# Optimization experiments

Hardware: AMD Instinct MI355X
Metric: run time of the kernel (lower is better)

The kernel has to match this reference:

```python
import jax, jax.numpy as jnp
import numpy as np

HIDDEN = 1024
KEY_DIM = 1280


def setup_inputs() -> dict:
    key = jax.random.key(0)
    ks = jax.random.split(key, 8)
    B, L = 32, 2048
    # Xavier-uniform style init for weights, bias = 0.01 (as in module)
    def xavier(k, shape):
        fan_in, fan_out = shape[1], shape[0]
        limit = float(np.sqrt(6.0 / (fan_in + fan_out)))
        return jax.random.uniform(k, shape, jnp.float32, -limit, limit)
    return {
        "query": jax.random.normal(ks[0], (B, HIDDEN), jnp.float32),
        "keys": jax.random.normal(ks[1], (B, L, KEY_DIM), jnp.float32),
        "W1_w": xavier(ks[2], (HIDDEN, HIDDEN)),
        "W1_b": jnp.full((HIDDEN,), 0.01, jnp.float32),
        "W2_w": xavier(ks[3], (HIDDEN, KEY_DIM)),
        "W2_b": jnp.full((HIDDEN,), 0.01, jnp.float32),
        "Va_w": xavier(ks[4], (1, HIDDEN)),
        "Va_b": jnp.full((1,), 0.01, jnp.float32),
    }


def reference(query, keys, W1_w, W1_b, W2_w, W2_b, Va_w, Va_b):
    # hidden: [B, H], encoder: [B, L, H]
    hidden = query @ W1_w.T + W1_b
    encoder = jnp.einsum("blk,hk->blh", keys, W2_w) + W2_b
    # additive score: Va(relu(hidden[:,None,:] + encoder)) -> [B, L]
    act = jax.nn.relu(hidden[:, None, :] + encoder)
    scores = jnp.einsum("blh,h->bl", act, Va_w[0]) + Va_b[0]
    weights = jax.nn.softmax(scores, axis=1)  # [B, L]
    context = jnp.einsum("blk,bl->bk", keys, weights)  # [B, KEY_DIM]
    return context, weights
```

## Files before the change

### kernel.cpp

```cpp
#include <hip/hip_runtime.h>
#include <hip/hip_bf16.h>
#include <cstdint>
#include <cstddef>

#define NB 32
#define NL 2048
#define NH 1024
#define NK 1280

typedef __bf16 bf16x8 __attribute__((ext_vector_type(8)));
typedef short short8 __attribute__((ext_vector_type(8)));
typedef float f32x4 __attribute__((ext_vector_type(4)));
typedef unsigned short u16x4 __attribute__((ext_vector_type(4)));
typedef unsigned short u16x8 __attribute__((ext_vector_type(8)));

__device__ __forceinline__ float bfbits2f(unsigned short b) {
    union { unsigned int u; float f; } v;
    v.u = ((unsigned int)b) << 16;
    return v.f;
}

__device__ __forceinline__ void load_lds16(const void* g, void* l) {
    __builtin_amdgcn_global_load_lds((const __attribute__((address_space(1))) void*)g,
                                     (__attribute__((address_space(3))) void*)l, 16, 0, 0);
}

__global__ __launch_bounds__(256) void k_w2cvt(const float* __restrict__ w2,
                                               unsigned short* __restrict__ w2b) {
    int i = (blockIdx.x * 256 + threadIdx.x) * 4;
    f32x4 v = *(const f32x4*)(w2 + i);
    u16x4 o;
#pragma unroll
    for (int c = 0; c < 4; ++c) {
        __bf16 b = (__bf16)v[c];
        o[c] = __builtin_bit_cast(unsigned short, b);
    }
    *(u16x4*)(w2b + i) = o;
}

__global__ __launch_bounds__(256) void k_keyscvt(const float* __restrict__ keys,
                                                 unsigned short* __restrict__ kb) {
    size_t i = ((size_t)blockIdx.x * 256 + threadIdx.x) * 8;
    f32x4 v0 = *(const f32x4*)(keys + i);
    f32x4 v1 = *(const f32x4*)(keys + i + 4);
    u16x8 o;
#pragma unroll
    for (int c = 0; c < 4; ++c) {
        o[c] = __builtin_bit_cast(unsigned short, (__bf16)v0[c]);
        o[c + 4] = __builtin_bit_cast(unsigned short, (__bf16)v1[c]);
    }
    *(u16x8*)(kb + i) = o;
}

__global__ __launch_bounds__(256) void k_hidden(const float* __restrict__ q,
                                                const float* __restrict__ w1,
                                                const float* __restrict__ w1b,
                                                const float* __restrict__ w2b,
                                                float* __restrict__ hidden) {
    const int t = threadIdx.x;
    const int h = blockIdx.x;
    __shared__ __align__(16) float w[1024];
    __shared__ float red[256];
    *(f32x4*)&w[t * 4] = *(const f32x4*)(w1 + (size_t)h * 1024 + t * 4);
    __syncthreads();
    const int b = t & 31, seg = t >> 5;
    const f32x4* q4 = (const f32x4*)(q + (size_t)b * 1024 + seg * 128);
    f32x4 accv = (f32x4){0.f, 0.f, 0.f, 0.f};
#pragma unroll 4
    for (int i = 0; i < 32; ++i) {
        f32x4 qv = q4[i];
        f32x4 wv = *(f32x4*)&w[seg * 128 + i * 4];
#pragma unroll
        for (int c = 0; c < 4; ++c) accv[c] = fmaf(qv[c], wv[c], accv[c]);
    }
    red[t] = accv[0] + accv[1] + accv[2] + accv[3];
    __syncthreads();
    if (t < 32) {
        float tot = 0.f;
#pragma unroll
        for (int sg = 0; sg < 8; ++sg) tot += red[sg * 32 + t];
        hidden[(size_t)t * 1024 + h] = tot + w1b[h] + w2b[h];
    }
}

__global__ __launch_bounds__(512, 2) void k_score_bf(const unsigned short* __restrict__ keysbf,
                                                     const unsigned short* __restrict__ w2bf,
                                                     const float* __restrict__ hidden,
                                                     const float* __restrict__ va,
                                                     float* __restrict__ spart) {
    __shared__ __align__(16) __bf16 As[32768];
    __shared__ __align__(16) __bf16 Bs[32768];
    __shared__ float sred[1024];

    const int t = threadIdx.x;
    const int lane = t & 63, wid = t >> 6;
    const int wr = wid >> 2, wc = wid & 3;
    const int pl = lane >> 4, r0 = lane & 15;

    const int bid = blockIdx.x;
    const int v = (bid & 7) * 128 + (bid >> 3);
    const int rt = v >> 2;
    const int ht = v & 3;

    const int b = rt >> 3;
    float hv[4], vav[4];
#pragma unroll
    for (int n = 0; n < 4; ++n) {
        int h = ht * 256 + wc * 64 + n * 16 + r0;
        hv[n] = hidden[(size_t)b * 1024 + h];
        vav[n] = va[h];
    }

    const int cj0 = wid * 2, cj1 = wid * 2 + 1;
    const unsigned short* pA0 = keysbf + (size_t)(rt * 256 + (cj0 & 3) * 64 + lane) * 1280 + (cj0 >> 2) * 8;
    const unsigned short* pA1 = keysbf + (size_t)(rt * 256 + (cj1 & 3) * 64 + lane) * 1280 + (cj1 >> 2) * 8;
    const unsigned short* pB0 = w2bf + (size_t)(ht * 256 + (cj0 & 3) * 64 + lane) * 1280 + (cj0 >> 2) * 8;
    const unsigned short* pB1 = w2bf + (size_t)(ht * 256 + (cj1 & 3) * 64 + lane) * 1280 + (cj1 >> 2) * 8;
    const int dst0 = cj0 * 1024 + lane * 16;
    const int dst1 = cj1 * 1024 + lane * 16;

    const int aBase = pl * 2048 + (wr * 128 + r0) * 8;
    const int bBase = pl * 2048 + (wc * 64 + r0) * 8;

    f32x4 acc[8][4];
#pragma unroll
    for (int m = 0; m < 8; ++m)
#pragma unroll
        for (int n = 0; n < 4; ++n) acc[m][n] = (f32x4){0.f, 0.f, 0.f, 0.f};
    bf16x8 bB[4];

#define ST_A(NXT, KOFF, KS)                                                          \
    do {                                                                             \
        load_lds16(pA0 + (KOFF) + (KS) * 32, (char*)As + (NXT) * 32768 + (KS) * 16384 + dst0); \
        load_lds16(pA1 + (KOFF) + (KS) * 32, (char*)As + (NXT) * 32768 + (KS) * 16384 + dst1); \
    } while (0)
#define ST_B(NXT, KOFF, KS)                                                          \
    do {                                                                             \
        load_lds16(pB0 + (KOFF) + (KS) * 32, (char*)Bs + (NXT) * 32768 + (KS) * 16384 + dst0); \
        load_lds16(pB1 + (KOFF) + (KS) * 32, (char*)Bs + (NXT) * 32768 + (KS) * 16384 + dst1); \
    } while (0)

#define PH(CUR, KS, MH, RDB, STMT, WAITN, TRAIL)                                     \
    do {                                                                             \
        if (RDB) {                                                                   \
            _Pragma("unroll") for (int n = 0; n < 4; ++n)                            \
                bB[n] = *(bf16x8*)&Bs[(CUR) * 16384 + (KS) * 8192 + bBase + n * 128];\
        }                                                                            \
        bf16x8 aT[4];                                                                \
        _Pragma("unroll") for (int mm = 0; mm < 4; ++mm)                             \
            aT[mm] = *(bf16x8*)&As[(CUR) * 16384 + (KS) * 8192 + aBase + (MH) * 512 + mm * 128]; \
        STMT;                                                                        \
        if ((WAITN) == 4) asm volatile("s_waitcnt vmcnt(4)" ::: "memory");           \
        else if ((WAITN) == 2) asm volatile("s_waitcnt vmcnt(2)" ::: "memory");      \
        else if ((WAITN) == 0) asm volatile("s_waitcnt vmcnt(0)" ::: "memory");      \
        __builtin_amdgcn_s_barrier();                                                \
        asm volatile("s_waitcnt lgkmcnt(0)" ::: "memory");                           \
        __builtin_amdgcn_sched_barrier(0);                                           \
        __builtin_amdgcn_s_setprio(1);                                               \
        _Pragma("unroll") for (int mm = 0; mm < 4; ++mm)                             \
            _Pragma("unroll") for (int n = 0; n < 4; ++n)                            \
                acc[(MH) * 4 + mm][n] = __builtin_amdgcn_mfma_f32_16x16x32_bf16(     \
                    aT[mm], bB[n], acc[(MH) * 4 + mm][n], 0, 0, 0);                  \
        __builtin_amdgcn_s_setprio(0);                                               \
        if (TRAIL) __builtin_amdgcn_s_barrier();                                     \
    } while (0)

#define TILE(CUR, NXT, KOFF, W2, W4, DOST)                                           \
    do {                                                                             \
        PH(CUR, 0, 0, 1, if (DOST) ST_A(NXT, KOFF, 0), -1, 0);                       \
        PH(CUR, 0, 1, 0, if (DOST) ST_A(NXT, KOFF, 1), W2, 0);                       \
        PH(CUR, 1, 0, 1, if (DOST) ST_B(NXT, KOFF, 0), -1, 0);                       \
        PH(CUR, 1, 1, 0, if (DOST) ST_B(NXT, KOFF, 1), W4, 1);                       \
    } while (0)

    ST_A(0, 0, 0);
    ST_A(0, 0, 1);
    ST_B(0, 0, 0);
    ST_B(0, 0, 1);
    asm volatile("s_waitcnt vmcnt(2)" ::: "memory");
    __builtin_amdgcn_s_barrier();

    int koff = 64;
    for (int t2 = 0; t2 < 9; ++t2) {
        TILE(0, 1, koff, 4, 2, 1);
        koff += 64;
        TILE(1, 0, koff, 4, 2, 1);
        koff += 64;
    }
    TILE(0, 1, koff, 4, 2, 1);
    TILE(1, 0, 0, 0, -1, 0);
#undef TILE
#undef PH
#undef ST_A
#undef ST_B

#pragma unroll
    for (int m = 0; m < 8; ++m) {
#pragma unroll
        for (int j = 0; j < 4; ++j) {
            float s = 0.f;
#pragma unroll
            for (int n = 0; n < 4; ++n) {
                float v2 = acc[m][n][j] + hv[n];
                v2 = fmaxf(v2, 0.f);
                s = fmaf(v2, vav[n], s);
            }
            s += __shfl_xor(s, 1);
            s += __shfl_xor(s, 2);
            s += __shfl_xor(s, 4);
            s += __shfl_xor(s, 8);
            if (r0 == 0) sred[(wr * 128 + m * 16 + pl * 4 + j) * 4 + wc] = s;
        }
    }
    __syncthreads();
    if (t < 256)
        spart[(size_t)ht * 65536 + rt * 256 + t] =
            (sred[t * 4] + sred[t * 4 + 1]) + (sred[t * 4 + 2] + sred[t * 4 + 3]);
}

#define LOAD_AB(IT)                                        \
    do {                                                   \
        const float* ap_ = aptr + (IT) * 32;               \
        a0 = *(const f32x4*)(ap_);                         \
        a1 = *(const f32x4*)(ap_ + 4);                     \
        a2 = *(const f32x4*)(ap_ + 8);                     \
        a3 = *(const f32x4*)(ap_ + 12);                    \
        const unsigned short* bp_ = bptr + (IT) * 32;      \
        b0 = *(const short8*)(bp_);                        \
        b1 = *(const short8*)(bp_ + 8);                    \
    } while (0)

__global__ __launch_bounds__(256, 2) void k_score_f32(const float* __restrict__ keys,
                                                      const unsigned short* __restrict__ w2bf,
                                                      const float* __restrict__ hidden,
                                                      const float* __restrict__ va,
                                                      float* __restrict__ spart) {
    __shared__ __align__(16) __bf16 As[4096];
    __shared__ __align__(16) __bf16 Bs[4096];
    __shared__ float sred[256];
    const int t = threadIdx.x;
    const int rt = blockIdx.x, ht = blockIdx.y;
    const int row = t >> 1, half = t & 1;
    const float* aptr = keys + (size_t)(rt * 128 + row) * 1280 + half * 16;
    const unsigned short* bptr = w2bf + (size_t)(ht * 128 + row) * 1280 + half * 16;
    const int wA0 = (2 * half) * 1024 + row * 8;
    const int wA1 = wA0 + 1024;
    f32x4 acc[4][4];
#pragma unroll
    for (int m = 0; m < 4; ++m)
#pragma unroll
        for (int n = 0; n < 4; ++n) acc[m][n] = (f32x4){0.f, 0.f, 0.f, 0.f};
    const int lane = t & 63, wid = t >> 6;
    const int wr = wid >> 1, wc = wid & 1;
    const int pl = lane >> 4, r0 = lane & 15;
    const int aroff = pl * 1024 + (wr * 64 + r0) * 8;
    const int broff = pl * 1024 + (wc * 64 + r0) * 8;
    f32x4 a0, a1, a2, a3;
    short8 b0, b1;
    LOAD_AB(0);
    for (int it = 0; it < 40; ++it) {
        __syncthreads();
        bf16x8 p0, p1;
#pragma unroll
        for (int e = 0; e < 4; ++e) {
            p0[e] = (__bf16)a0[e];
            p0[e + 4] = (__bf16)a1[e];
            p1[e] = (__bf16)a2[e];
            p1[e + 4] = (__bf16)a3[e];
        }
        *(bf16x8*)&As[wA0] = p0;
        *(bf16x8*)&As[wA1] = p1;
        *(short8*)&Bs[wA0] = b0;
        *(short8*)&Bs[wA1] = b1;
        __syncthreads();
        if (it + 1 < 40) LOAD_AB(it + 1);
        bf16x8 af[4], bfv[4];
#pragma unroll
        for (int m = 0; m < 4; ++m) af[m] = *(bf16x8*)&As[aroff + m * 128];
#pragma unroll
        for (int n = 0; n < 4; ++n) bfv[n] = *(bf16x8*)&Bs[broff + n * 128];
#pragma unroll
        for (int m = 0; m < 4; ++m)
#pragma unroll
            for (int n = 0; n < 4; ++n)
                acc[m][n] = __builtin_amdgcn_mfma_f32_16x16x32_bf16(af[m], bfv[n], acc[m][n], 0, 0, 0);
    }
    const int b = rt >> 4;
    float hv[4], vav[4];
#pragma unroll
    for (int n = 0; n < 4; ++n) {
        int h = ht * 128 + wc * 64 + n * 16 + r0;
        hv[n] = hidden[(size_t)b * 1024 + h];
        vav[n] = va[h];
    }
#pragma unroll
    for (int m = 0; m < 4; ++m) {
#pragma unroll
        for (int j = 0; j < 4; ++j) {
            float s = 0.f;
#pragma unroll
            for (int n = 0; n < 4; ++n) {
                float v = acc[m][n][j] + hv[n];
                v = fmaxf(v, 0.f);
                s = fmaf(v, vav[n], s);
            }
            s += __shfl_xor(s, 1);
            s += __shfl_xor(s, 2);
            s += __shfl_xor(s, 4);
            s += __shfl_xor(s, 8);
            if (r0 == 0) sred[(wr * 64 + m * 16 + pl * 4 + j) * 2 + wc] = s;
        }
    }
    __syncthreads();
    if (t < 128) spart[(size_t)ht * 65536 + rt * 128 + t] = sred[t * 2] + sred[t * 2 + 1];
}

__global__ __launch_bounds__(256) void k_softmax4(const float* __restrict__ spart,
                                                  float* __restrict__ wout) {
    const int b = blockIdx.x, t = threadIdx.x;
    __shared__ float red[256];
    float s[8];
#pragma unroll
    for (int i = 0; i < 8; ++i) {
        int l = t + i * 256;
        float v = 0.f;
#pragma unroll
        for (int ht = 0; ht < 4; ++ht) v += spart[(size_t)ht * 65536 + b * 2048 + l];
        s[i] = v;
    }
    float mx = s[0];
#pragma unroll
    for (int i = 1; i < 8; ++i) mx = fmaxf(mx, s[i]);
    red[t] = mx;
    __syncthreads();
    for (int st = 128; st > 0; st >>= 1) {
        if (t < st) red[t] = fmaxf(red[t], red[t + st]);
        __syncthreads();
    }
    mx = red[0];
    __syncthreads();
    float e[8];
    float sum = 0.f;
#pragma unroll
    for (int i = 0; i < 8; ++i) {
        e[i] = __expf(s[i] - mx);
        sum += e[i];
    }
    red[t] = sum;
    __syncthreads();
    for (int st = 128; st > 0; st >>= 1) {
        if (t < st) red[t] += red[t + st];
        __syncthreads();
    }
    float inv = 1.0f / red[0];
#pragma unroll
    for (int i = 0; i < 8; ++i) wout[(size_t)b * 2048 + t + i * 256] = e[i] * inv;
}

__global__ __launch_bounds__(256) void k_softmax8(const float* __restrict__ spart,
                                                  float* __restrict__ wout) {
    const int b = blockIdx.x, t = threadIdx.x;
    __shared__ float red[256];
    float s[8];
#pragma unroll
    for (int i = 0; i < 8; ++i) {
        int l = t + i * 256;
        float v = 0.f;
#pragma unroll
        for (int ht = 0; ht < 8; ++ht) v += spart[(size_t)ht * 65536 + b * 2048 + l];
        s[i] = v;
    }
    float mx = s[0];
#pragma unroll
    for (int i = 1; i < 8; ++i) mx = fmaxf(mx, s[i]);
    red[t] = mx;
    __syncthreads();
    for (int st = 128; st > 0; st >>= 1) {
        if (t < st) red[t] = fmaxf(red[t], red[t + st]);
        __syncthreads();
    }
    mx = red[0];
    __syncthreads();
    float e[8];
    float sum = 0.f;
#pragma unroll
    for (int i = 0; i < 8; ++i) {
        e[i] = __expf(s[i] - mx);
        sum += e[i];
    }
    red[t] = sum;
    __syncthreads();
    for (int st = 128; st > 0; st >>= 1) {
        if (t < st) red[t] += red[t + st];
        __syncthreads();
    }
    float inv = 1.0f / red[0];
#pragma unroll
    for (int i = 0; i < 8; ++i) wout[(size_t)b * 2048 + t + i * 256] = e[i] * inv;
}

__global__ __launch_bounds__(256) void k_ctx_bf(const unsigned short* __restrict__ keysbf,
                                                const float* __restrict__ wts,
                                                float* __restrict__ cpart) {
    const int b = blockIdx.x, kc = blockIdx.y, lc = blockIdx.z, t = threadIdx.x;
    const int c = t & 15, g = t >> 4;
    const unsigned short* kp = keysbf + ((size_t)b * 2048 + lc * 512 + g) * 1280 + kc * 128 + c * 8;
    const float* wb = wts + (size_t)b * 2048 + lc * 512 + g;
    float acc[8];
#pragma unroll
    for (int j = 0; j < 8; ++j) acc[j] = 0.f;
    for (int i = 0; i < 32; ++i) {
        u16x8 v = *(const u16x8*)kp;
        float w = *wb;
#pragma unroll
        for (int j = 0; j < 8; ++j) acc[j] = fmaf(w, bfbits2f(v[j]), acc[j]);
        kp += (size_t)16 * 1280;
        wb += 16;
    }
    __shared__ float sred[2048];
#pragma unroll
    for (int j = 0; j < 8; ++j) sred[t * 8 + j] = acc[j];
    __syncthreads();
    if (t < 128) {
        float s = 0.f;
#pragma unroll
        for (int g2 = 0; g2 < 16; ++g2) s += sred[g2 * 128 + t];
        cpart[((size_t)lc * 32 + b) * 1280 + kc * 128 + t] = s;
    }
}

__global__ __launch_bounds__(256) void k_ctxred4(const float* __restrict__ cpart,
                                                 float* __restrict__ ctx) {
    const int idx = blockIdx.x * 256 + threadIdx.x;
    const int b = idx / 1280, k = idx % 1280;
    float s = 0.f;
#pragma unroll
    for (int lc = 0; lc < 4; ++lc) s += cpart[((size_t)lc * 32 + b) * 1280 + k];
    ctx[(size_t)b * 1280 + k] = s;
}

__global__ __launch_bounds__(256) void k_ctxpart_f32(const float* __restrict__ keys,
                                                     const float* __restrict__ wts,
                                                     float* __restrict__ cpart) {
    const int b = blockIdx.x, lc = blockIdx.y, t = threadIdx.x;
    f32x4 acc0 = (f32x4){0.f, 0.f, 0.f, 0.f};
    f32x4 acc1 = (f32x4){0.f, 0.f, 0.f, 0.f};
    const int l0 = lc * 128;
    const float* kb = keys + ((size_t)b * 2048 + l0) * 1280;
    const float* wb = wts + (size_t)b * 2048 + l0;
    for (int l = 0; l < 128; ++l) {
        float w = wb[l];
        const f32x4* kr = (const f32x4*)(kb + (size_t)l * 1280);
        f32x4 v = kr[t];
#pragma unroll
        for (int ci = 0; ci < 4; ++ci) acc0[ci] = fmaf(v[ci], w, acc0[ci]);
        if (t < 64) {
            f32x4 v2 = kr[256 + t];
#pragma unroll
            for (int ci = 0; ci < 4; ++ci) acc1[ci] = fmaf(v2[ci], w, acc1[ci]);
        }
    }
    float* cp = cpart + ((size_t)lc * 32 + b) * 1280;
    *(f32x4*)(cp + 4 * t) = acc0;
    if (t < 64) *(f32x4*)(cp + 1024 + 4 * t) = acc1;
}

__global__ __launch_bounds__(256) void k_ctxred16(const float* __restrict__ cpart,
                                                  float* __restrict__ ctx) {
    const int idx = blockIdx.x * 256 + threadIdx.x;
    const int b = idx / 1280, k = idx % 1280;
    float s = 0.f;
#pragma unroll
    for (int lc = 0; lc < 16; ++lc) s += cpart[((size_t)lc * 32 + b) * 1280 + k];
    ctx[(size_t)b * 1280 + k] = s;
}

extern "C" void kernel_launch(void* const* d_in, const int* in_sizes, int n_in,
                              void* d_out, int out_size, void* d_ws, size_t ws_size,
                              hipStream_t stream) {
    const float* query = (const float*)d_in[0];
    const float* keys = (const float*)d_in[1];
    const float* W1_w = (const float*)d_in[2];
    const float* W1_b = (const float*)d_in[3];
    const float* W2_w = (const float*)d_in[4];
    const float* W2_b = (const float*)d_in[5];
    const float* Va_w = (const float*)d_in[6];

    float* out = (float*)d_out;
    float* ctx = out;
    float* wts = out + NB * NK;

    char* ws = (char*)d_ws;
    float* hidden = (float*)ws;
    unsigned short* w2bf = (unsigned short*)(ws + 131072);
    float* spart = (float*)(ws + 2752512);
    float* cpart = (float*)(ws + 4849664);
    unsigned short* keysbf = (unsigned short*)(ws + 7471104);
    const bool big = ws_size >= (size_t)7471104 + 167772160;

    k_w2cvt<<<1280, 256, 0, stream>>>(W2_w, w2bf);
    k_hidden<<<1024, 256, 0, stream>>>(query, W1_w, W1_b, W2_b, hidden);
    if (big) {
        k_keyscvt<<<40960, 256, 0, stream>>>(keys, keysbf);
        k_score_bf<<<1024, 512, 0, stream>>>(keysbf, w2bf, hidden, Va_w, spart);
        k_softmax4<<<32, 256, 0, stream>>>(spart, wts);
        k_ctx_bf<<<dim3(32, 10, 4), 256, 0, stream>>>(keysbf, wts, cpart);
        k_ctxred4<<<160, 256, 0, stream>>>(cpart, ctx);
    } else {
        k_score_f32<<<dim3(512, 8), 256, 0, stream>>>(keys, w2bf, hidden, Va_w, spart);
        k_softmax8<<<32, 256, 0, stream>>>(spart, wts);
        k_ctxpart_f32<<<dim3(32, 16), 256, 0, stream>>>(keys, wts, cpart);
        k_ctxred16<<<160, 256, 0, stream>>>(cpart, ctx);
    }
}
```

Baseline: 395.6 us.

## Replace four-phase barrier pipeline with one barrier per K tile

```diff
diff --git a/kernel.cpp b/kernel.cpp
--- a/kernel.cpp
+++ b/kernel.cpp
@@ -127,7 +127,6 @@
     for (int m = 0; m < 8; ++m)
 #pragma unroll
         for (int n = 0; n < 4; ++n) acc[m][n] = (f32x4){0.f, 0.f, 0.f, 0.f};
-    bf16x8 bB[4];
 
 #define ST_A(NXT, KOFF, KS)                                                          \
     do {                                                                             \
@@ -140,57 +139,64 @@
         load_lds16(pB1 + (KOFF) + (KS) * 32, (char*)Bs + (NXT) * 32768 + (KS) * 16384 + dst1); \
     } while (0)
 
-#define PH(CUR, KS, MH, RDB, STMT, WAITN, TRAIL)                                     \
+#define RD_B(DST, CUR, KS)                                                           \
+    _Pragma("unroll") for (int n = 0; n < 4; ++n)                                    \
+        DST[n] = *(bf16x8*)&Bs[(CUR) * 16384 + (KS) * 8192 + bBase + n * 128];
+#define RD_A(DST, CUR, KS, MH)                                                       \
+    _Pragma("unroll") for (int mm = 0; mm < 4; ++mm)                                 \
+        DST[mm] = *(bf16x8*)&As[(CUR) * 16384 + (KS) * 8192 + aBase + (MH) * 512 + mm * 128];
+#define MM(AV, BV, MH)                                                               \
     do {                                                                             \
-        if (RDB) {                                                                   \
-            _Pragma("unroll") for (int n = 0; n < 4; ++n)                            \
-                bB[n] = *(bf16x8*)&Bs[(CUR) * 16384 + (KS) * 8192 + bBase + n * 128];\
-        }                                                                            \
-        bf16x8 aT[4];                                                                \
-        _Pragma("unroll") for (int mm = 0; mm < 4; ++mm)                             \
-            aT[mm] = *(bf16x8*)&As[(CUR) * 16384 + (KS) * 8192 + aBase + (MH) * 512 + mm * 128]; \
-        STMT;                                                                        \
-        if ((WAITN) == 4) asm volatile("s_waitcnt vmcnt(4)" ::: "memory");           \
-        else if ((WAITN) == 2) asm volatile("s_waitcnt vmcnt(2)" ::: "memory");      \
-        else if ((WAITN) == 0) asm volatile("s_waitcnt vmcnt(0)" ::: "memory");      \
-        __builtin_amdgcn_s_barrier();                                                \
-        asm volatile("s_waitcnt lgkmcnt(0)" ::: "memory");                           \
-        __builtin_amdgcn_sched_barrier(0);                                           \
         __builtin_amdgcn_s_setprio(1);                                               \
         _Pragma("unroll") for (int mm = 0; mm < 4; ++mm)                             \
             _Pragma("unroll") for (int n = 0; n < 4; ++n)                            \
                 acc[(MH) * 4 + mm][n] = __builtin_amdgcn_mfma_f32_16x16x32_bf16(     \
-                    aT[mm], bB[n], acc[(MH) * 4 + mm][n], 0, 0, 0);                  \
+                    AV[mm], BV[n], acc[(MH) * 4 + mm][n], 0, 0, 0);                  \
         __builtin_amdgcn_s_setprio(0);                                               \
-        if (TRAIL) __builtin_amdgcn_s_barrier();                                     \
     } while (0)
 
-#define TILE(CUR, NXT, KOFF, W2, W4, DOST)                                           \
+#define TILE(CUR, NXT, KOFF, DOST, LAST)                                             \
     do {                                                                             \
-        PH(CUR, 0, 0, 1, if (DOST) ST_A(NXT, KOFF, 0), -1, 0);                       \
-        PH(CUR, 0, 1, 0, if (DOST) ST_A(NXT, KOFF, 1), W2, 0);                       \
-        PH(CUR, 1, 0, 1, if (DOST) ST_B(NXT, KOFF, 0), -1, 0);                       \
-        PH(CUR, 1, 1, 0, if (DOST) ST_B(NXT, KOFF, 1), W4, 1);                       \
+        if (DOST) { ST_A(NXT, KOFF, 0); ST_A(NXT, KOFF, 1); }                        \
+        bf16x8 b0v[4], ax[4], ay[4];                                                 \
+        RD_B(b0v, CUR, 0);                                                           \
+        RD_A(ax, CUR, 0, 0);                                                         \
+        RD_A(ay, CUR, 0, 1);                                                         \
+        MM(ax, b0v, 0);                                                              \
+        MM(ay, b0v, 1);                                                              \
+        if (DOST) { ST_B(NXT, KOFF, 0); ST_B(NXT, KOFF, 1); }                        \
+        bf16x8 b1v[4], ax2[4], ay2[4];                                               \
+        RD_B(b1v, CUR, 1);                                                           \
+        RD_A(ax2, CUR, 1, 0);                                                        \
+        RD_A(ay2, CUR, 1, 1);                                                        \
+        MM(ax2, b1v, 0);                                                             \
+        MM(ay2, b1v, 1);                                                             \
+        if (!(LAST)) {                                                               \
+            asm volatile("s_waitcnt vmcnt(0)" ::: "memory");                         \
+            __builtin_amdgcn_s_barrier();                                            \
+        }                                                                            \
     } while (0)
 
     ST_A(0, 0, 0);
     ST_A(0, 0, 1);
     ST_B(0, 0, 0);
     ST_B(0, 0, 1);
-    asm volatile("s_waitcnt vmcnt(2)" ::: "memory");
+    asm volatile("s_waitcnt vmcnt(0)" ::: "memory");
     __builtin_amdgcn_s_barrier();
 
     int koff = 64;
     for (int t2 = 0; t2 < 9; ++t2) {
-        TILE(0, 1, koff, 4, 2, 1);
+        TILE(0, 1, koff, 1, 0);
         koff += 64;
-        TILE(1, 0, koff, 4, 2, 1);
+        TILE(1, 0, koff, 1, 0);
         koff += 64;
     }
-    TILE(0, 1, koff, 4, 2, 1);
-    TILE(1, 0, 0, 0, -1, 0);
+    TILE(0, 1, koff, 1, 0);
+    TILE(1, 0, 0, 0, 1);
 #undef TILE
-#undef PH
+#undef MM
+#undef RD_A
+#undef RD_B
 #undef ST_A
 #undef ST_B
 
```

Measured after the change: 397.1 us. Within noise of the previous version (+0.4%).

## Restructure GEMM mainloop into 4-stage K=32 LDS pipeline with XOR swizzle

Applied to the files above, without the earlier changes.

```diff
diff --git a/kernel.cpp b/kernel.cpp
--- a/kernel.cpp
+++ b/kernel.cpp
@@ -111,88 +111,80 @@
         vav[n] = va[h];
     }
 
-    const int cj0 = wid * 2, cj1 = wid * 2 + 1;
-    const unsigned short* pA0 = keysbf + (size_t)(rt * 256 + (cj0 & 3) * 64 + lane) * 1280 + (cj0 >> 2) * 8;
-    const unsigned short* pA1 = keysbf + (size_t)(rt * 256 + (cj1 & 3) * 64 + lane) * 1280 + (cj1 >> 2) * 8;
-    const unsigned short* pB0 = w2bf + (size_t)(ht * 256 + (cj0 & 3) * 64 + lane) * 1280 + (cj0 >> 2) * 8;
-    const unsigned short* pB1 = w2bf + (size_t)(ht * 256 + (cj1 & 3) * 64 + lane) * 1280 + (cj1 >> 2) * 8;
-    const int dst0 = cj0 * 1024 + lane * 16;
-    const int dst1 = cj1 * 1024 + lane * 16;
-
-    const int aBase = pl * 2048 + (wr * 128 + r0) * 8;
-    const int bBase = pl * 2048 + (wc * 64 + r0) * 8;
+    const int srow = wid * 32 + (lane >> 2);
+    const int sseg = (lane & 3) ^ ((lane >> 3) & 3);
+    const unsigned short* pA = keysbf + (size_t)(rt * 256 + srow) * 1280 + sseg * 8;
+    const unsigned short* pB = w2bf + (size_t)(ht * 256 + srow) * 1280 + sseg * 8;
+    const int sdst = wid * 2048 + lane * 16;
+
+    const int slotSw = (pl ^ ((r0 >> 1) & 3)) * 8;
+    const int aBase = (wr * 128 + r0) * 32 + slotSw;
+    const int bBase = (wc * 64 + r0) * 32 + slotSw;
 
     f32x4 acc[8][4];
 #pragma unroll
     for (int m = 0; m < 8; ++m)
 #pragma unroll
         for (int n = 0; n < 4; ++n) acc[m][n] = (f32x4){0.f, 0.f, 0.f, 0.f};
-    bf16x8 bB[4];
-
-#define ST_A(NXT, KOFF, KS)                                                          \
+
+#define STAGE(STBUF, KOFF)                                                           \
     do {                                                                             \
-        load_lds16(pA0 + (KOFF) + (KS) * 32, (char*)As + (NXT) * 32768 + (KS) * 16384 + dst0); \
-        load_lds16(pA1 + (KOFF) + (KS) * 32, (char*)As + (NXT) * 32768 + (KS) * 16384 + dst1); \
+        load_lds16(pA + (KOFF), (char*)As + (STBUF) * 16384 + sdst);                 \
+        load_lds16(pA + (KOFF) + 16 * 1280, (char*)As + (STBUF) * 16384 + sdst + 1024); \
+        load_lds16(pB + (KOFF), (char*)Bs + (STBUF) * 16384 + sdst);                 \
+        load_lds16(pB + (KOFF) + 16 * 1280, (char*)Bs + (STBUF) * 16384 + sdst + 1024); \
     } while (0)
-#define ST_B(NXT, KOFF, KS)                                                          \
+
+#define TILE(BUF, STBUF, DOST, WAITN)                                                \
     do {                                                                             \
-        load_lds16(pB0 + (KOFF) + (KS) * 32, (char*)Bs + (NXT) * 32768 + (KS) * 16384 + dst0); \
-        load_lds16(pB1 + (KOFF) + (KS) * 32, (char*)Bs + (NXT) * 32768 + (KS) * 16384 + dst1); \
-    } while (0)
-
-#define PH(CUR, KS, MH, RDB, STMT, WAITN, TRAIL)                                     \
-    do {                                                                             \
-        if (RDB) {                                                                   \
-            _Pragma("unroll") for (int n = 0; n < 4; ++n)                            \
-                bB[n] = *(bf16x8*)&Bs[(CUR) * 16384 + (KS) * 8192 + bBase + n * 128];\
-        }                                                                            \
-        bf16x8 aT[4];                                                                \
+        if (DOST) { STAGE(STBUF, koff); koff += 32; }                                \
+        bf16x8 bv[4], a0v[4], a1v[4];                                                \
+        _Pragma("unroll") for (int n = 0; n < 4; ++n)                                \
+            bv[n] = *(bf16x8*)&Bs[(BUF) * 8192 + bBase + n * 512];                   \
         _Pragma("unroll") for (int mm = 0; mm < 4; ++mm)                             \
-            aT[mm] = *(bf16x8*)&As[(CUR) * 16384 + (KS) * 8192 + aBase + (MH) * 512 + mm * 128]; \
-        STMT;                                                                        \
-        if ((WAITN) == 4) asm volatile("s_waitcnt vmcnt(4)" ::: "memory");           \
-        else if ((WAITN) == 2) asm volatile("s_waitcnt vmcnt(2)" ::: "memory");      \
-        else if ((WAITN) == 0) asm volatile("s_waitcnt vmcnt(0)" ::: "memory");      \
-        __builtin_amdgcn_s_barrier();                                                \
-        asm volatile("s_waitcnt lgkmcnt(0)" ::: "memory");                           \
-        __builtin_amdgcn_sched_barrier(0);                                           \
+            a0v[mm] = *(bf16x8*)&As[(BUF) * 8192 + aBase + mm * 512];                 \
         __builtin_amdgcn_s_setprio(1);                                               \
         _Pragma("unroll") for (int mm = 0; mm < 4; ++mm)                             \
             _Pragma("unroll") for (int n = 0; n < 4; ++n)                            \
-                acc[(MH) * 4 + mm][n] = __builtin_amdgcn_mfma_f32_16x16x32_bf16(     \
-                    aT[mm], bB[n], acc[(MH) * 4 + mm][n], 0, 0, 0);                  \
+                acc[mm][n] = __builtin_amdgcn_mfma_f32_16x16x32_bf16(                \
+                    a0v[mm], bv[n], acc[mm][n], 0, 0, 0);                            \
         __builtin_amdgcn_s_setprio(0);                                               \
-        if (TRAIL) __builtin_amdgcn_s_barrier();                                     \
+        _Pragma("unroll") for (int mm = 0; mm < 4; ++mm)                             \
+            a1v[mm] = *(bf16x8*)&As[(BUF) * 8192 + aBase + 2048 + mm * 512];          \
+        __builtin_amdgcn_s_setprio(1);                                               \
+        _Pragma("unroll") for (int mm = 0; mm < 4; ++mm)                             \
+            _Pragma("unroll") for (int n = 0; n < 4; ++n)                            \
+                acc[4 + mm][n] = __builtin_amdgcn_mfma_f32_16x16x32_bf16(            \
+                    a1v[mm], bv[n], acc[4 + mm][n], 0, 0, 0);                        \
+        __builtin_amdgcn_s_setprio(0);                                               \
+        if ((WAITN) == 4) {                                                          \
+            asm volatile("s_waitcnt vmcnt(4)" ::: "memory");                         \
+            __builtin_amdgcn_s_barrier();                                            \
+        } else if ((WAITN) == 0) {                                                   \
+            asm volatile("s_waitcnt vmcnt(0)" ::: "memory");                         \
+            __builtin_amdgcn_s_barrier();                                            \
+        }                                                                            \
     } while (0)
 
-#define TILE(CUR, NXT, KOFF, W2, W4, DOST)                                           \
-    do {                                                                             \
-        PH(CUR, 0, 0, 1, if (DOST) ST_A(NXT, KOFF, 0), -1, 0);                       \
-        PH(CUR, 0, 1, 0, if (DOST) ST_A(NXT, KOFF, 1), W2, 0);                       \
-        PH(CUR, 1, 0, 1, if (DOST) ST_B(NXT, KOFF, 0), -1, 0);                       \
-        PH(CUR, 1, 1, 0, if (DOST) ST_B(NXT, KOFF, 1), W4, 1);                       \
-    } while (0)
-
-    ST_A(0, 0, 0);
-    ST_A(0, 0, 1);
-    ST_B(0, 0, 0);
-    ST_B(0, 0, 1);
-    asm volatile("s_waitcnt vmcnt(2)" ::: "memory");
+    int koff = 0;
+    STAGE(0, 0);
+    STAGE(1, 32);
+    koff = 64;
+    asm volatile("s_waitcnt vmcnt(4)" ::: "memory");
     __builtin_amdgcn_s_barrier();
 
-    int koff = 64;
-    for (int t2 = 0; t2 < 9; ++t2) {
-        TILE(0, 1, koff, 4, 2, 1);
-        koff += 64;
-        TILE(1, 0, koff, 4, 2, 1);
-        koff += 64;
-    }
-    TILE(0, 1, koff, 4, 2, 1);
-    TILE(1, 0, 0, 0, -1, 0);
+    for (int i = 0; i < 9; ++i) {
+        TILE(0, 2, 1, 4);
+        TILE(1, 3, 1, 4);
+        TILE(2, 0, 1, 4);
+        TILE(3, 1, 1, 4);
+    }
+    TILE(0, 2, 1, 4);
+    TILE(1, 3, 1, 4);
+    TILE(2, 0, 0, 0);
+    TILE(3, 0, 0, -1);
 #undef TILE
-#undef PH
-#undef ST_A
-#undef ST_B
+#undef STAGE
 
 #pragma unroll
     for (int m = 0; m < 8; ++m) {
```

New measurement: 326.8 us. -17.4%, faster.
